# Kernel tuning notes

Measured on AMD Instinct MI355X. Metric: run time of the kernel, lower is better.

The kernel has to match this reference:

```python
import jax, jax.numpy as jnp
import numpy as np

N_NODES = 65536
N_EDGES = 524288
N_GRAPHS = 64
PTS_PER_GRAPH = 1024


def gcn_conv(x, W, b, row, col, self_idx, n_nodes):
    # PyG GCNConv: x' = D^{-1/2} (A + I) D^{-1/2} x W + b
    xw = x @ W
    row2 = jnp.concatenate([row, self_idx])
    col2 = jnp.concatenate([col, self_idx])
    deg = jax.ops.segment_sum(jnp.ones_like(col2, dtype=xw.dtype), col2, num_segments=n_nodes)
    dinv = jax.lax.rsqrt(deg)  # deg >= 1 thanks to self-loops
    norm = dinv[row2] * dinv[col2]  # [E+N]
    out = jax.ops.segment_sum(xw[row2] * norm[:, None], col2, num_segments=n_nodes)
    return out + b


def setup_inputs() -> dict:
    key = jax.random.key(0)
    ks = jax.random.split(key, 12)

    def glorot(k, fan_in, fan_out):
        s = jnp.sqrt(6.0 / (fan_in + fan_out))
        return jax.random.uniform(k, (fan_in, fan_out), jnp.float32, -s, s)

    x = jax.random.normal(ks[0], (N_NODES, 3), jnp.float32)
    edge_index = jax.random.randint(ks[1], (2, N_EDGES), 0, N_NODES, dtype=jnp.int64)
    batch = (jnp.arange(N_NODES, dtype=jnp.int64) // PTS_PER_GRAPH)  # 64 graphs x 1024 pts

    return {
        "x": x, "edge_index": edge_index, "batch": batch,
        "W1": glorot(ks[2], 3, 64), "b1": jnp.zeros((64,), jnp.float32),
        "W2": glorot(ks[3], 64, 256), "b2": jnp.zeros((256,), jnp.float32),
        "W3": glorot(ks[4], 256, 512), "b3": jnp.zeros((512,), jnp.float32),
        "Wm1": glorot(ks[5], 1024, 512), "bm1": jnp.zeros((512,), jnp.float32),
        "Wm2": glorot(ks[6], 512, 10), "bm2": jnp.zeros((10,), jnp.float32),
    }


def reference(x, edge_index, batch, W1, b1, W2, b2, W3, b3, Wm1, bm1, Wm2, bm2):
    n = x.shape[0]
    row, col = edge_index[0], edge_index[1]
    self_idx = jnp.arange(n, dtype=edge_index.dtype)

    x1 = jax.nn.relu(gcn_conv(x, W1, b1, row, col, self_idx, n))
    x2 = jax.nn.relu(gcn_conv(x1, W2, b2, row, col, self_idx, n))
    x3 = jax.nn.relu(gcn_conv(x2, W3, b3, row, col, self_idx, n))

    # global mean / max pool over batch segments
    counts = jax.ops.segment_sum(jnp.ones((n,), x3.dtype), batch, num_segments=N_GRAPHS)
    x_mean = jax.ops.segment_sum(x3, batch, num_segments=N_GRAPHS) / counts[:, None]
    x_max = jax.ops.segment_max(x3, batch, num_segments=N_GRAPHS)
    h = jnp.concatenate([x_mean, x_max], axis=1)  # [G, 1024]

    h = jax.nn.relu(h @ Wm1 + bm1)  # dropout is identity in eval
    return h @ Wm2 + bm2  # [G, 10]
```

## Files before the change

### kernel.cpp

```cpp
#include <hip/hip_runtime.h>
#include <hip/hip_bf16.h>

typedef __hip_bfloat16 bf16;
typedef short bf16x8 __attribute__((ext_vector_type(8)));
typedef float f32x4 __attribute__((ext_vector_type(4)));
typedef unsigned int u32x4 __attribute__((ext_vector_type(4)));

__device__ __forceinline__ float b2f_us(unsigned short u) {
    union { unsigned int i; float f; } c;
    c.i = ((unsigned int)u) << 16;
    return c.f;
}
__device__ __forceinline__ unsigned short f2b_us(float f) {
    bf16 h = __float2bfloat16(f);
    return *reinterpret_cast<unsigned short*>(&h);
}
__device__ __forceinline__ void unpack8(uint4 p, float* f) {
    f[0] = b2f_us(p.x & 0xffff); f[1] = b2f_us(p.x >> 16);
    f[2] = b2f_us(p.y & 0xffff); f[3] = b2f_us(p.y >> 16);
    f[4] = b2f_us(p.z & 0xffff); f[5] = b2f_us(p.z >> 16);
    f[6] = b2f_us(p.w & 0xffff); f[7] = b2f_us(p.w >> 16);
}

__device__ __forceinline__ void async_copy16(const bf16* g, bf16* l) {
    __builtin_amdgcn_global_load_lds(
        (const __attribute__((address_space(1))) unsigned int*)g,
        (__attribute__((address_space(3))) unsigned int*)l, 16, 0, 0);
}

__global__ __launch_bounds__(256) void k_count(const int* __restrict__ col,
                                               int* __restrict__ cnt,
                                               int* __restrict__ rank, int E) {
    int e = blockIdx.x * 256 + threadIdx.x;
    if (e < E) rank[e] = atomicAdd(cnt + col[e], 1);
}
__global__ __launch_bounds__(256) void k_scan_a(const int* __restrict__ cnt,
                                                int* __restrict__ bsum,
                                                float* __restrict__ dinv) {
    __shared__ int s[256];
    int t = threadIdx.x;
    int i = blockIdx.x * 256 + t;
    int c = cnt[i];
    dinv[i] = rsqrtf((float)c + 1.0f);
    s[t] = c;
    __syncthreads();
#pragma unroll
    for (int off = 128; off >= 1; off >>= 1) {
        if (t < off) s[t] += s[t + off];
        __syncthreads();
    }
    if (t == 0) bsum[blockIdx.x] = s[0];
}
__global__ __launch_bounds__(256) void k_scan_c(const int* __restrict__ cnt,
                                                const int* __restrict__ bsum,
                                                int* __restrict__ rowptr) {
    __shared__ int s[256];
    __shared__ int sb[256];
    int t = threadIdx.x;
    sb[t] = bsum[t];
    __syncthreads();
#pragma unroll
    for (int off = 1; off < 256; off <<= 1) {
        int v = (t >= off) ? sb[t - off] : 0;
        __syncthreads();
        sb[t] += v;
        __syncthreads();
    }
    int boff = (blockIdx.x > 0) ? sb[blockIdx.x - 1] : 0;
    int base = blockIdx.x * 256;
    int self = cnt[base + t];
    s[t] = self;
    __syncthreads();
#pragma unroll
    for (int off = 1; off < 256; off <<= 1) {
        int v = (t >= off) ? s[t - off] : 0;
        __syncthreads();
        s[t] += v;
        __syncthreads();
    }
    rowptr[base + t] = boff + s[t] - self;
}

__global__ __launch_bounds__(256) void k_scatter(const int* __restrict__ row,
                                                 const int* __restrict__ col,
                                                 const float* __restrict__ dinv,
                                                 const int* __restrict__ rowptr,
                                                 const int* __restrict__ rank,
                                                 int2* __restrict__ adj, int E) {
    int e = blockIdx.x * 256 + threadIdx.x;
    if (e >= E) return;
    int r = row[e], c = col[e];
    int pos = rowptr[c] + rank[e];
    adj[pos] = make_int2(r, __float_as_int(dinv[r]));
}

__global__ __launch_bounds__(256) void k_prep_all(const float* __restrict__ W2,
                                                  bf16* __restrict__ WT2,
                                                  const float* __restrict__ W3,
                                                  bf16* __restrict__ WT3) {
    int idx = blockIdx.x * 256 + threadIdx.x;
    if (idx < 64 * 256) {
        int k = idx >> 8, n = idx & 255;
        WT2[n * 64 + k] = __float2bfloat16(W2[idx]);
    } else {
        int i = idx - 64 * 256;
        if (i < 256 * 512) {
            int k = i >> 9, n = i & 511;
            WT3[(size_t)n * 256 + k] = __float2bfloat16(W3[i]);
        }
    }
}

__global__ __launch_bounds__(256) void k_gcn1(const int2* __restrict__ adj,
                                              const int* __restrict__ rowptr,
                                              const int* __restrict__ cnt,
                                              const float* __restrict__ dinv,
                                              const float* __restrict__ x,
                                              const float* __restrict__ W,
                                              const float* __restrict__ bias,
                                              bf16* __restrict__ h1, int N) {
    __shared__ float w[256];
    int t = threadIdx.x;
    if (t < 192) w[t] = W[t];
    else w[t] = bias[t - 192];
    __syncthreads();
    int node = blockIdx.x * 64 + (t >> 2);
    int q = t & 3;
    if (node >= N) return;
    float d = dinv[node];
    float a0 = 0.f, a1 = 0.f, a2 = 0.f;
    if (q == 0) {
        float d2 = d * d;
        a0 = x[node * 3] * d2;
        a1 = x[node * 3 + 1] * d2;
        a2 = x[node * 3 + 2] * d2;
    }
    int beg = rowptr[node], deg = cnt[node];
    int e   = beg + (deg * q) / 4;
    int end = beg + (deg * (q + 1)) / 4;
    for (; e + 3 < end; e += 4) {
        int2 ad[4];
#pragma unroll
        for (int u = 0; u < 4; ++u) ad[u] = adj[e + u];
        float xv[4][3];
#pragma unroll
        for (int u = 0; u < 4; ++u) {
            xv[u][0] = x[ad[u].x * 3];
            xv[u][1] = x[ad[u].x * 3 + 1];
            xv[u][2] = x[ad[u].x * 3 + 2];
        }
#pragma unroll
        for (int u = 0; u < 4; ++u) {
            float wt = __int_as_float(ad[u].y) * d;
            a0 += xv[u][0] * wt;
            a1 += xv[u][1] * wt;
            a2 += xv[u][2] * wt;
        }
    }
    for (; e < end; ++e) {
        int2 ad = adj[e];
        float wt = __int_as_float(ad.y) * d;
        a0 += x[ad.x * 3] * wt;
        a1 += x[ad.x * 3 + 1] * wt;
        a2 += x[ad.x * 3 + 2] * wt;
    }
    a0 += __shfl_xor(a0, 1); a1 += __shfl_xor(a1, 1); a2 += __shfl_xor(a2, 1);
    a0 += __shfl_xor(a0, 2); a1 += __shfl_xor(a1, 2); a2 += __shfl_xor(a2, 2);
    bf16* dst = h1 + (size_t)node * 64;
#pragma unroll
    for (int i = 0; i < 2; ++i) {
        int fb = q + 4 * i;
        uint4 r;
        unsigned v[4];
#pragma unroll
        for (int p = 0; p < 4; ++p) {
            int f0 = fb * 8 + p * 2;
            float u0 = fmaxf(a0 * w[f0] + a1 * w[64 + f0] + a2 * w[128 + f0] + w[192 + f0], 0.f);
            int f1 = f0 + 1;
            float u1 = fmaxf(a0 * w[f1] + a1 * w[64 + f1] + a2 * w[128 + f1] + w[192 + f1], 0.f);
            v[p] = (unsigned)f2b_us(u0) | ((unsigned)f2b_us(u1) << 16);
        }
        r.x = v[0]; r.y = v[1]; r.z = v[2]; r.w = v[3];
        *reinterpret_cast<uint4*>(dst + fb * 8) = r;
    }
}

__global__ __launch_bounds__(512, 4) void k_gcn2(const int2* __restrict__ adj,
                                                 const int* __restrict__ rowptr,
                                                 const int* __restrict__ cnt,
                                                 const float* __restrict__ dinv,
                                                 const bf16* __restrict__ h1,
                                                 const bf16* __restrict__ WT2,
                                                 const float* __restrict__ bias,
                                                 bf16* __restrict__ h2, int N) {
    __shared__ bf16 As[64 * 64];
    __shared__ bf16 Bs[256 * 64];
    const int t = threadIdx.x;
    const int m0 = blockIdx.x * 64;
#pragma unroll
    for (int i = 0; i < 4; ++i) {
        int c = i * 512 + t;
        int n = c >> 3, q = c & 7;
        int qs = q ^ (n & 7);
        async_copy16(WT2 + n * 64 + qs * 8, Bs + c * 8);
    }
    {
        const int gi = t >> 4, gl = t & 15;
        const int fs = gl & 7, half = gl >> 3;
        const int fbase = fs * 8;
#pragma unroll 1
        for (int p = 0; p < 2; ++p) {
            int r = p * 32 + gi;
            int node = m0 + r;
            float d = dinv[node];
            float a[8] = {0.f, 0.f, 0.f, 0.f, 0.f, 0.f, 0.f, 0.f};
            if (half == 0) {
                uint4 sp = *reinterpret_cast<const uint4*>(h1 + (size_t)node * 64 + fbase);
                unpack8(sp, a);
                float d2 = d * d;
#pragma unroll
                for (int i = 0; i < 8; i++) a[i] *= d2;
            }
            int beg = rowptr[node], deg = cnt[node];
            int mid = beg + ((deg + 1) >> 1);
            int e = half ? mid : beg;
            int end = half ? (beg + deg) : mid;
            for (; e + 3 < end; e += 4) {
                int2 ad[4];
                uint4 pl[4];
#pragma unroll
                for (int u = 0; u < 4; ++u) ad[u] = adj[e + u];
#pragma unroll
                for (int u = 0; u < 4; ++u)
                    pl[u] = *reinterpret_cast<const uint4*>(h1 + (size_t)ad[u].x * 64 + fbase);
#pragma unroll
                for (int u = 0; u < 4; ++u) {
                    float wt = __int_as_float(ad[u].y) * d;
                    float f[8];
                    unpack8(pl[u], f);
#pragma unroll
                    for (int i = 0; i < 8; i++) a[i] += f[i] * wt;
                }
            }
            for (; e < end; ++e) {
                int2 ad = adj[e];
                float wt = __int_as_float(ad.y) * d;
                uint4 pl = *reinterpret_cast<const uint4*>(h1 + (size_t)ad.x * 64 + fbase);
                float f[8];
                unpack8(pl, f);
#pragma unroll
                for (int i = 0; i < 8; i++) a[i] += f[i] * wt;
            }
#pragma unroll
            for (int i = 0; i < 8; i++) a[i] += __shfl_xor(a[i], 8);
            if (half == 0) {
                u32x4 rr;
                rr.x = (unsigned)f2b_us(a[0]) | ((unsigned)f2b_us(a[1]) << 16);
                rr.y = (unsigned)f2b_us(a[2]) | ((unsigned)f2b_us(a[3]) << 16);
                rr.z = (unsigned)f2b_us(a[4]) | ((unsigned)f2b_us(a[5]) << 16);
                rr.w = (unsigned)f2b_us(a[6]) | ((unsigned)f2b_us(a[7]) << 16);
                int q = fs ^ (r & 7);
                *reinterpret_cast<u32x4*>(&As[r * 64 + q * 8]) = rr;
            }
        }
    }
    __syncthreads();
    const int w = t >> 6, lane = t & 63;
    const int quad = lane >> 4, l16 = lane & 15;
    const int wmq = w & 3, wnh = w >> 2;
    f32x4 acc[8] = {};
#pragma unroll
    for (int kb = 0; kb < 2; ++kb) {
        int R = wmq * 16 + l16;
        int kc = kb * 4 + quad;
        bf16x8 af = *reinterpret_cast<const bf16x8*>(&As[R * 64 + (kc ^ (R & 7)) * 8]);
#pragma unroll
        for (int j = 0; j < 8; ++j) {
            int n = wnh * 128 + j * 16 + l16;
            bf16x8 bfr = *reinterpret_cast<const bf16x8*>(&Bs[n * 64 + (kc ^ (n & 7)) * 8]);
            acc[j] = __builtin_amdgcn_mfma_f32_16x16x32_bf16(af, bfr, acc[j], 0, 0, 0);
        }
    }
#pragma unroll
    for (int j = 0; j < 8; ++j) {
        int cn = wnh * 128 + j * 16 + l16;
        float bv = bias[cn];
#pragma unroll
        for (int r = 0; r < 4; ++r) {
            int row = m0 + wmq * 16 + quad * 4 + r;
            h2[(size_t)row * 256 + cn] = __float2bfloat16(fmaxf(acc[j][r] + bv, 0.f));
        }
    }
}

template <int F>
__global__ __launch_bounds__(256, 8) void k_gather_pre(const int2* __restrict__ adj,
                                                       const int* __restrict__ rowptr,
                                                       const int* __restrict__ cnt,
                                                       const float* __restrict__ dinv,
                                                       const bf16* __restrict__ h,
                                                       bf16* __restrict__ agg, int N) {
    constexpr int LPN = F / 8;
    constexpr int GRP = 2 * LPN;
    constexpr int NPB = 256 / GRP;
    int t = threadIdx.x;
    int node = blockIdx.x * NPB + t / GRP;
    if (node >= N) return;
    int gl = t % GRP;
    int fs = gl % LPN;
    int half = gl / LPN;
    int fbase = fs * 8;
    float d = dinv[node];
    size_t sbase = (size_t)node * F + fbase;
    float a[8] = {0.f, 0.f, 0.f, 0.f, 0.f, 0.f, 0.f, 0.f};
    if (half == 0) {
        uint4 sp = *reinterpret_cast<const uint4*>(h + sbase);
        unpack8(sp, a);
        float d2 = d * d;
#pragma unroll
        for (int i = 0; i < 8; i++) a[i] *= d2;
    }
    int beg = rowptr[node];
    int deg = cnt[node];
    int mid = beg + ((deg + 1) >> 1);
    int e   = half ? mid : beg;
    int end = half ? (beg + deg) : mid;
    for (; e + 3 < end; e += 4) {
        int2 ad[4];
        uint4 p[4];
#pragma unroll
        for (int u = 0; u < 4; ++u) ad[u] = adj[e + u];
#pragma unroll
        for (int u = 0; u < 4; ++u)
            p[u] = *reinterpret_cast<const uint4*>(h + (size_t)ad[u].x * F + fbase);
#pragma unroll
        for (int u = 0; u < 4; ++u) {
            float wt = __int_as_float(ad[u].y) * d;
            float f[8];
            unpack8(p[u], f);
#pragma unroll
            for (int i = 0; i < 8; i++) a[i] += f[i] * wt;
        }
    }
    for (; e < end; ++e) {
        int2 ad = adj[e];
        float wt = __int_as_float(ad.y) * d;
        uint4 p = *reinterpret_cast<const uint4*>(h + (size_t)ad.x * F + fbase);
        float f[8];
        unpack8(p, f);
#pragma unroll
        for (int i = 0; i < 8; i++) a[i] += f[i] * wt;
    }
#pragma unroll
    for (int i = 0; i < 8; i++) a[i] += __shfl_xor(a[i], LPN);
    if (half == 0) {
        u32x4 r;
        r.x = (unsigned)f2b_us(a[0]) | ((unsigned)f2b_us(a[1]) << 16);
        r.y = (unsigned)f2b_us(a[2]) | ((unsigned)f2b_us(a[3]) << 16);
        r.z = (unsigned)f2b_us(a[4]) | ((unsigned)f2b_us(a[5]) << 16);
        r.w = (unsigned)f2b_us(a[6]) | ((unsigned)f2b_us(a[7]) << 16);
        __builtin_nontemporal_store(r, reinterpret_cast<u32x4*>(agg + sbase));
    }
}

__global__ __launch_bounds__(256) void k_gemm_pool(const bf16* __restrict__ A,
                                                   const bf16* __restrict__ BT,
                                                   const float* __restrict__ bias,
                                                   float* __restrict__ partials,
                                                   int M, int N, int K) {
    __shared__ bf16 As[128 * 32];
    __shared__ bf16 Bs[128 * 32];
    const int t = threadIdx.x;
    const int wave = t >> 6, lane = t & 63;
    const int quad = lane >> 4, l16 = lane & 15;
    const int wm = wave & 1, wn = wave >> 1;
    const int L = blockIdx.x;
    const int xcd = L & 7, slot = L >> 3;
    const int mt = xcd * 64 + (slot >> 2), nt = slot & 3;
    const int m0 = mt * 128;
    const int n0 = nt * 128;

    f32x4 acc[4][4] = {};
    for (int kb = 0; kb < K; kb += 32) {
#pragma unroll
        for (int rnd = 0; rnd < 2; ++rnd) {
            int c = (rnd * 4 + wave) * 64 + lane;
            int r = c >> 2, seg = c & 3;
            async_copy16(A + (size_t)(m0 + r) * K + kb + seg * 8, As + c * 8);
            async_copy16(BT + (size_t)(n0 + r) * K + kb + seg * 8, Bs + c * 8);
        }
        __syncthreads();
        bf16x8 af[4], bfr[4];
#pragma unroll
        for (int i = 0; i < 4; i++)
            af[i] = *reinterpret_cast<const bf16x8*>(&As[(wm * 64 + i * 16 + l16) * 32 + quad * 8]);
#pragma unroll
        for (int j = 0; j < 4; j++)
            bfr[j] = *reinterpret_cast<const bf16x8*>(&Bs[(wn * 64 + j * 16 + l16) * 32 + quad * 8]);
#pragma unroll
        for (int i = 0; i < 4; i++)
#pragma unroll
            for (int j = 0; j < 4; j++)
                acc[i][j] = __builtin_amdgcn_mfma_f32_16x16x32_bf16(af[i], bfr[j], acc[i][j], 0, 0, 0);
        __syncthreads();
    }
    size_t pbase = ((size_t)(mt * 4 + nt) * 2 + wm) * 256;
#pragma unroll
    for (int j = 0; j < 4; j++) {
        int f128 = wn * 64 + j * 16 + l16;
        float bv = bias[n0 + f128];
        float s = 0.f, mx = 0.f;
#pragma unroll
        for (int i = 0; i < 4; i++)
#pragma unroll
            for (int r = 0; r < 4; r++) {
                float v = fmaxf(acc[i][j][r] + bv, 0.f);
                s += v;
                mx = fmaxf(mx, v);
            }
        s += __shfl_xor(s, 16);
        s += __shfl_xor(s, 32);
        mx = fmaxf(mx, __shfl_xor(mx, 16));
        mx = fmaxf(mx, __shfl_xor(mx, 32));
        if (quad == 0) {
            partials[pbase + f128] = s;
            partials[pbase + 128 + f128] = mx;
        }
    }
}

__global__ __launch_bounds__(256) void k_mlp1(const float* __restrict__ partials,
                                              const float* __restrict__ Wm1,
                                              const float* __restrict__ bm1,
                                              float* __restrict__ o) {
    __shared__ float hg[1024];
    __shared__ float red[256];
    int g = blockIdx.x;
    int t = threadIdx.x;
    for (int ff = t; ff < 512; ff += 256) {
        int by = ff >> 7, f128 = ff & 127;
        float S = 0.f, M = 0.f;
#pragma unroll
        for (int tile = 0; tile < 8; ++tile) {
            int bx = g * 8 + tile;
#pragma unroll
            for (int wm = 0; wm < 2; ++wm) {
                size_t pbase = ((size_t)(bx * 4 + by) * 2 + wm) * 256;
                S += partials[pbase + f128];
                M = fmaxf(M, partials[pbase + 128 + f128]);
            }
        }
        hg[ff] = S * (1.0f / 1024.0f);
        hg[512 + ff] = M;
    }
    __syncthreads();
    int f64 = t & 63, kq = t >> 6;
    int f = blockIdx.y * 64 + f64;
    float acc = 0.f;
    int k0 = kq * 256;
#pragma unroll 8
    for (int k = k0; k < k0 + 256; ++k)
        acc += hg[k] * Wm1[(size_t)k * 512 + f];
    red[t] = acc;
    __syncthreads();
    if (t < 64) {
        float total = red[t] + red[t + 64] + red[t + 128] + red[t + 192] + bm1[f];
        o[g * 512 + f] = fmaxf(total, 0.f);
    }
}

__global__ __launch_bounds__(512) void k_mlp2(const float* __restrict__ h,
                                              const float* __restrict__ Wm2,
                                              const float* __restrict__ bm2,
                                              float* __restrict__ out) {
    int g = blockIdx.x;
    int t = threadIdx.x;
    int j = t >> 5, lane32 = t & 31;
    float acc = 0.f;
    if (j < 10) {
        int k0 = lane32 * 16;
#pragma unroll
        for (int i = 0; i < 16; ++i)
            acc += h[g * 512 + k0 + i] * Wm2[(size_t)(k0 + i) * 10 + j];
    }
#pragma unroll
    for (int m = 16; m >= 1; m >>= 1) acc += __shfl_xor(acc, m);
    if (j < 10 && lane32 == 0) out[g * 10 + j] = acc + bm2[j];
}

extern "C" void kernel_launch(void* const* d_in, const int* in_sizes, int n_in,
                              void* d_out, int out_size, void* d_ws, size_t ws_size,
                              hipStream_t stream) {
    const float* x   = (const float*)d_in[0];
    const int*   ei  = (const int*)d_in[1];
    const float* W1  = (const float*)d_in[3];
    const float* b1  = (const float*)d_in[4];
    const float* W2  = (const float*)d_in[5];
    const float* b2  = (const float*)d_in[6];
    const float* W3  = (const float*)d_in[7];
    const float* b3  = (const float*)d_in[8];
    const float* Wm1 = (const float*)d_in[9];
    const float* bm1 = (const float*)d_in[10];
    const float* Wm2 = (const float*)d_in[11];
    const float* bm2 = (const float*)d_in[12];
    float* out = (float*)d_out;

    const int N = in_sizes[0] / 3;
    const int E = in_sizes[1] / 2;
    const int* row = ei;
    const int* col = ei + E;

    char* ws = (char*)d_ws;
    size_t off = 0;
    auto alloc = [&](size_t bytes) {
        void* p = ws + off;
        off += (bytes + 255) & ~(size_t)255;
        return p;
    };
    int*   cnt      = (int*)alloc((size_t)N * 4);
    int*   rowptr   = (int*)alloc((size_t)N * 4);
    float* dinv     = (float*)alloc((size_t)N * 4);
    int*   bsum     = (int*)alloc(256 * 4);
    int*   rank     = (int*)alloc((size_t)E * 4);
    int2*  adj      = (int2*)alloc((size_t)E * 8);
    bf16*  h1       = (bf16*)alloc((size_t)N * 64 * 2);
    bf16*  h2       = (bf16*)alloc((size_t)N * 256 * 2);
    bf16*  agg3     = (bf16*)alloc((size_t)N * 256 * 2);
    bf16*  WT2      = (bf16*)alloc(256 * 64 * 2);
    bf16*  WT3      = (bf16*)alloc(512 * 256 * 2);
    float* partials = (float*)alloc((size_t)512 * 4 * 2 * 256 * 4);
    float* m1       = (float*)alloc(64 * 512 * 4);

    (void)hipMemsetAsync(cnt, 0, (size_t)N * 4, stream);
    k_count<<<(E + 255) / 256, 256, 0, stream>>>(col, cnt, rank, E);
    k_scan_a<<<256, 256, 0, stream>>>(cnt, bsum, dinv);
    k_scan_c<<<256, 256, 0, stream>>>(cnt, bsum, rowptr);
    k_scatter<<<(E + 255) / 256, 256, 0, stream>>>(row, col, dinv, rowptr, rank, adj, E);

    k_prep_all<<<(64 * 256 + 256 * 512 + 255) / 256, 256, 0, stream>>>(W2, WT2, W3, WT3);

    k_gcn1<<<N / 64, 256, 0, stream>>>(adj, rowptr, cnt, dinv, x, W1, b1, h1, N);

    k_gcn2<<<N / 64, 512, 0, stream>>>(adj, rowptr, cnt, dinv, h1, WT2, b2, h2, N);

    k_gather_pre<256><<<(N * 64) / 256, 256, 0, stream>>>(adj, rowptr, cnt, dinv, h2, agg3, N);
    k_gemm_pool<<<(N / 128) * 4, 256, 0, stream>>>(agg3, WT3, b3, partials, N, 512, 256);

    k_mlp1<<<dim3(64, 8), 256, 0, stream>>>(partials, Wm1, bm1, m1);
    k_mlp2<<<64, 512, 0, stream>>>(m1, Wm2, bm2, out);
}
```

Baseline: 245.9 us.

## Enlarge pooled GEMM tiles to 256x256 and fuse the two MLP kernels

New measurement: 281.8 us. 1.15x slower.

```diff
diff --git a/kernel.cpp b/kernel.cpp
--- a/kernel.cpp
+++ b/kernel.cpp
@@ -363,55 +363,52 @@
     }
 }
 
-__global__ __launch_bounds__(256) void k_gemm_pool(const bf16* __restrict__ A,
+__global__ __launch_bounds__(512) void k_gemm_pool(const bf16* __restrict__ A,
                                                    const bf16* __restrict__ BT,
                                                    const float* __restrict__ bias,
                                                    float* __restrict__ partials,
                                                    int M, int N, int K) {
-    __shared__ bf16 As[128 * 32];
-    __shared__ bf16 Bs[128 * 32];
+    __shared__ bf16 As[256 * 32];
+    __shared__ bf16 Bs[256 * 32];
     const int t = threadIdx.x;
     const int wave = t >> 6, lane = t & 63;
     const int quad = lane >> 4, l16 = lane & 15;
     const int wm = wave & 1, wn = wave >> 1;
-    const int L = blockIdx.x;
-    const int xcd = L & 7, slot = L >> 3;
-    const int mt = xcd * 64 + (slot >> 2), nt = slot & 3;
-    const int m0 = mt * 128;
-    const int n0 = nt * 128;
-
-    f32x4 acc[4][4] = {};
+    const int mt = blockIdx.x >> 1, nt = blockIdx.x & 1;
+    const int m0 = mt * 256, n0 = nt * 256;
+
+    f32x4 acc[8][4] = {};
     for (int kb = 0; kb < K; kb += 32) {
 #pragma unroll
         for (int rnd = 0; rnd < 2; ++rnd) {
-            int c = (rnd * 4 + wave) * 64 + lane;
+            int c = rnd * 512 + t;
             int r = c >> 2, seg = c & 3;
             async_copy16(A + (size_t)(m0 + r) * K + kb + seg * 8, As + c * 8);
             async_copy16(BT + (size_t)(n0 + r) * K + kb + seg * 8, Bs + c * 8);
         }
         __syncthreads();
-        bf16x8 af[4], bfr[4];
-#pragma unroll
-        for (int i = 0; i < 4; i++)
-            af[i] = *reinterpret_cast<const bf16x8*>(&As[(wm * 64 + i * 16 + l16) * 32 + quad * 8]);
+        bf16x8 af[8], bfr[4];
+#pragma unroll
+        for (int i = 0; i < 8; i++)
+            af[i] = *reinterpret_cast<const bf16x8*>(&As[(wm * 128 + i * 16 + l16) * 32 + quad * 8]);
 #pragma unroll
         for (int j = 0; j < 4; j++)
             bfr[j] = *reinterpret_cast<const bf16x8*>(&Bs[(wn * 64 + j * 16 + l16) * 32 + quad * 8]);
 #pragma unroll
-        for (int i = 0; i < 4; i++)
+        for (int i = 0; i < 8; i++)
 #pragma unroll
             for (int j = 0; j < 4; j++)
                 acc[i][j] = __builtin_amdgcn_mfma_f32_16x16x32_bf16(af[i], bfr[j], acc[i][j], 0, 0, 0);
         __syncthreads();
     }
-    size_t pbase = ((size_t)(mt * 4 + nt) * 2 + wm) * 256;
+    size_t pbase = (size_t)(mt * 2 + wm) * 1024;
 #pragma unroll
     for (int j = 0; j < 4; j++) {
-        int f128 = wn * 64 + j * 16 + l16;
-        float bv = bias[n0 + f128];
+        int f = wn * 64 + j * 16 + l16;
+        float bv = bias[n0 + f];
         float s = 0.f, mx = 0.f;
 #pragma unroll
-        for (int i = 0; i < 4; i++)
+        for (int i = 0; i < 8; i++)
 #pragma unroll
             for (int r = 0; r < 4; r++) {
                 float v = fmaxf(acc[i][j][r] + bv, 0.f);
@@ -423,69 +420,58 @@
         mx = fmaxf(mx, __shfl_xor(mx, 16));
         mx = fmaxf(mx, __shfl_xor(mx, 32));
         if (quad == 0) {
-            partials[pbase + f128] = s;
-            partials[pbase + 128 + f128] = mx;
-        }
-    }
-}
-
-__global__ __launch_bounds__(256) void k_mlp1(const float* __restrict__ partials,
-                                              const float* __restrict__ Wm1,
-                                              const float* __restrict__ bm1,
-                                              float* __restrict__ o) {
+            partials[pbase + n0 + f] = s;
+            partials[pbase + 512 + n0 + f] = mx;
+        }
+    }
+}
+
+__global__ __launch_bounds__(256) void k_mlp(const float* __restrict__ partials,
+                                             const float* __restrict__ Wm1,
+                                             const float* __restrict__ bm1,
+                                             const float* __restrict__ Wm2,
+                                             const float* __restrict__ bm2,
+                                             float* __restrict__ out) {
     __shared__ float hg[1024];
-    __shared__ float red[256];
+    __shared__ float m2[512];
     int g = blockIdx.x;
     int t = threadIdx.x;
     for (int ff = t; ff < 512; ff += 256) {
-        int by = ff >> 7, f128 = ff & 127;
         float S = 0.f, M = 0.f;
 #pragma unroll
-        for (int tile = 0; tile < 8; ++tile) {
-            int bx = g * 8 + tile;
-#pragma unroll
-            for (int wm = 0; wm < 2; ++wm) {
-                size_t pbase = ((size_t)(bx * 4 + by) * 2 + wm) * 256;
-                S += partials[pbase + f128];
-                M = fmaxf(M, partials[pbase + 128 + f128]);
-            }
+        for (int k = 0; k < 8; ++k) {
+            size_t pbase = (size_t)(g * 8 + k) * 1024;
+            S += partials[pbase + ff];
+            M = fmaxf(M, partials[pbase + 512 + ff]);
         }
         hg[ff] = S * (1.0f / 1024.0f);
         hg[512 + ff] = M;
     }
     __syncthreads();
-    int f64 = t & 63, kq = t >> 6;
-    int f = blockIdx.y * 64 + f64;
-    float acc = 0.f;
-    int k0 = kq * 256;
-#pragma unroll 8
-    for (int k = k0; k < k0 + 256; ++k)
-        acc += hg[k] * Wm1[(size_t)k * 512 + f];
-    red[t] = acc;
-    __syncthreads();
-    if (t < 64) {
-        float total = red[t] + red[t + 64] + red[t + 128] + red[t + 192] + bm1[f];
-        o[g * 512 + f] = fmaxf(total, 0.f);
-    }
-}
-
-__global__ __launch_bounds__(512) void k_mlp2(const float* __restrict__ h,
-                                              const float* __restrict__ Wm2,
-                                              const float* __restrict__ bm2,
-                                              float* __restrict__ out) {
-    int g = blockIdx.x;
-    int t = threadIdx.x;
-    int j = t >> 5, lane32 = t & 31;
+#pragma unroll 1
+    for (int fo = 0; fo < 2; ++fo) {
+        int f = fo * 256 + t;
+        float a0 = 0.f, a1 = 0.f, a2 = 0.f, a3 = 0.f;
+        for (int k = 0; k < 1024; k += 4) {
+            a0 += hg[k]     * Wm1[(size_t)k * 512 + f];
+            a1 += hg[k + 1] * Wm1[(size_t)(k + 1) * 512 + f];
+            a2 += hg[k + 2] * Wm1[(size_t)(k + 2) * 512 + f];
+            a3 += hg[k + 3] * Wm1[(size_t)(k + 3) * 512 + f];
+        }
+        m2[f] = fmaxf(a0 + a1 + a2 + a3 + bm1[f], 0.f);
+    }
+    __syncthreads();
+    int j = t >> 4, l = t & 15;
     float acc = 0.f;
     if (j < 10) {
-        int k0 = lane32 * 16;
-#pragma unroll
-        for (int i = 0; i < 16; ++i)
-            acc += h[g * 512 + k0 + i] * Wm2[(size_t)(k0 + i) * 10 + j];
-    }
-#pragma unroll
-    for (int m = 16; m >= 1; m >>= 1) acc += __shfl_xor(acc, m);
-    if (j < 10 && lane32 == 0) out[g * 10 + j] = acc + bm2[j];
+        int k0 = l * 32;
+#pragma unroll
+        for (int i = 0; i < 32; ++i)
+            acc += m2[k0 + i] * Wm2[(size_t)(k0 + i) * 10 + j];
+    }
+#pragma unroll
+    for (int m = 8; m >= 1; m >>= 1) acc += __shfl_xor(acc, m);
+    if (j < 10 && l == 0) out[g * 10 + j] = acc + bm2[j];
 }
 
 extern "C" void kernel_launch(void* const* d_in, const int* in_sizes, int n_in,
@@ -528,8 +514,9 @@
     bf16*  agg3     = (bf16*)alloc((size_t)N * 256 * 2);
     bf16*  WT2      = (bf16*)alloc(256 * 64 * 2);
     bf16*  WT3      = (bf16*)alloc(512 * 256 * 2);
-    float* partials = (float*)alloc((size_t)512 * 4 * 2 * 256 * 4);
+    float* partials = (float*)alloc((size_t)512 * 1024 * 4);
     float* m1       = (float*)alloc(64 * 512 * 4);
+    (void)m1;
 
     (void)hipMemsetAsync(cnt, 0, (size_t)N * 4, stream);
     k_count<<<(E + 255) / 256, 256, 0, stream>>>(col, cnt, rank, E);
@@ -544,8 +531,7 @@
     k_gcn2<<<N / 64, 512, 0, stream>>>(adj, rowptr, cnt, dinv, h1, WT2, b2, h2, N);
 
     k_gather_pre<256><<<(N * 64) / 256, 256, 0, stream>>>(adj, rowptr, cnt, dinv, h2, agg3, N);
-    k_gemm_pool<<<(N / 128) * 4, 256, 0, stream>>>(agg3, WT3, b3, partials, N, 512, 256);
-
-    k_mlp1<<<dim3(64, 8), 256, 0, stream>>>(partials, Wm1, bm1, m1);
-    k_mlp2<<<64, 512, 0, stream>>>(m1, Wm2, bm2, out);
-}
+    k_gemm_pool<<<(N / 256) * 2, 512, 0, stream>>>(agg3, WT3, b3, partials, N, 512, 256);
+
+    k_mlp<<<64, 256, 0, stream>>>(partials, Wm1, bm1, Wm2, bm2, out);
+}
```
